# Optimization experiments

Measured on AMD Instinct MI355X. Metric: run time of the kernel, lower is better.

## Reference

```python
import jax, jax.numpy as jnp
import numpy as np

B, T, D_IN = 64, 1024, 400
H = 128            # hidden_dim_1 // 2 per direction
HD1, HD2 = 256, 64
N_CLASS, CONTEXT = 2, 2
EPS = 1e-5


def _lstm_dir(xs, w_ih, w_hh, b_ih, b_hh, reverse):
    # xs: [T, B, D]; torch gate order i, f, g, o
    Bd = xs.shape[1]
    def step(carry, xt):
        h, c = carry
        g = xt @ w_ih.T + b_ih + h @ w_hh.T + b_hh
        i, f, gg, o = jnp.split(g, 4, axis=-1)
        c = jax.nn.sigmoid(f) * c + jax.nn.sigmoid(i) * jnp.tanh(gg)
        h = jax.nn.sigmoid(o) * jnp.tanh(c)
        return (h, c), h
    init = (jnp.zeros((Bd, H), xs.dtype), jnp.zeros((Bd, H), xs.dtype))
    _, hs = jax.lax.scan(step, init, xs, reverse=reverse)
    return hs  # [T, B, H] in original time order


def _bn(x, g, b, m, v):  # eval-mode BatchNorm1d over last axis
    return (x - m) * jax.lax.rsqrt(v + EPS) * g + b


def _forward(x, w_ih_l0, w_hh_l0, b_ih_l0, b_hh_l0, w_ih_l0r, w_hh_l0r, b_ih_l0r, b_hh_l0r,
             w_ih_l1, w_hh_l1, b_ih_l1, b_hh_l1, w_ih_l1r, w_hh_l1r, b_ih_l1r, b_hh_l1r,
             bn1_g, bn1_b, bn1_m, bn1_v, lin_w, lin_b, bn2_g, bn2_b, bn2_m, bn2_v,
             out_w, out_b):
    xs = jnp.transpose(x, (1, 0, 2))  # [T, B, D_IN]
    # layer 0 bidirectional
    h_f = _lstm_dir(xs, w_ih_l0, w_hh_l0, b_ih_l0, b_hh_l0, False)
    h_b = _lstm_dir(xs, w_ih_l0r, w_hh_l0r, b_ih_l0r, b_hh_l0r, True)
    xs = jnp.concatenate([h_f, h_b], axis=-1)  # [T, B, 256]
    # layer 1 bidirectional
    h_f = _lstm_dir(xs, w_ih_l1, w_hh_l1, b_ih_l1, b_hh_l1, False)
    h_b = _lstm_dir(xs, w_ih_l1r, w_hh_l1r, b_ih_l1r, b_hh_l1r, True)
    lstm_out = jnp.concatenate([h_f, h_b], axis=-1)  # [T, B, 256]
    h = _bn(lstm_out, bn1_g, bn1_b, bn1_m, bn1_v)
    h = jnp.tanh(h @ lin_w.T + lin_b)
    h = _bn(h, bn2_g, bn2_b, bn2_m, bn2_v)  # [T, B, 64]
    # (equal x_len == T), so it is a per-batch scan with zero initial context
    def step(c, ht):  # c: [B, CONTEXT*N_CLASS], ht: [B, HD2]
        logits = jnp.concatenate([c, ht], axis=-1) @ out_w.T + out_b
        lo = jax.nn.log_softmax(logits, axis=-1)
        c_new = jax.lax.stop_gradient(jnp.concatenate([c[:, N_CLASS:], lo], axis=-1))
        return c_new, lo
    c0 = jnp.zeros((B, CONTEXT * N_CLASS), x.dtype)
    _, los = jax.lax.scan(step, c0, h)  # [T, B, N_CLASS]
    # torch flattens batch-major: row i = b * T + t
    return jnp.transpose(los, (1, 0, 2)).reshape(B * T, N_CLASS)


def setup_inputs() -> dict:
    keys = iter(jax.random.split(jax.random.key(0), 64))
    def u(shape):
        return jax.random.uniform(next(keys), shape, jnp.float32, -0.1, 0.1)
    inp = {"x": jax.random.normal(next(keys), (B, T, D_IN), jnp.float32)}
    for l, din in ((0, D_IN), (1, HD1)):
        for suf in ("", "r"):
            inp[f"w_ih_l{l}{suf}"] = u((4 * H, din))
            inp[f"w_hh_l{l}{suf}"] = u((4 * H, H))
            inp[f"b_ih_l{l}{suf}"] = u((4 * H,))
            inp[f"b_hh_l{l}{suf}"] = u((4 * H,))
    inp["bn1_g"] = u((HD1,)) + 1.0
    inp["bn1_b"] = u((HD1,))
    inp["bn1_m"] = u((HD1,))
    inp["bn1_v"] = jax.random.uniform(next(keys), (HD1,), jnp.float32, 0.5, 1.5)
    inp["lin_w"] = u((HD2, HD1))
    inp["lin_b"] = u((HD2,))
    inp["bn2_g"] = u((HD2,)) + 1.0
    inp["bn2_b"] = u((HD2,))
    inp["bn2_m"] = u((HD2,))
    inp["bn2_v"] = jax.random.uniform(next(keys), (HD2,), jnp.float32, 0.5, 1.5)
    inp["out_w"] = u((N_CLASS, CONTEXT * N_CLASS + HD2))
    inp["out_b"] = u((N_CLASS,))
    inp["x_len"] = jnp.full((B,), T, jnp.int32)
    return inp


def reference(x, w_ih_l0, w_hh_l0, b_ih_l0, b_hh_l0, w_ih_l0r, w_hh_l0r, b_ih_l0r, b_hh_l0r,
              w_ih_l1, w_hh_l1, b_ih_l1, b_hh_l1, w_ih_l1r, w_hh_l1r, b_ih_l1r, b_hh_l1r,
              bn1_g, bn1_b, bn1_m, bn1_v, lin_w, lin_b, bn2_g, bn2_b, bn2_m, bn2_v,
              out_w, out_b, x_len):
    # x_len is all-T (full-length sequences); packing is then a no-op and the
    # class_context reset indices coincide with sequence starts.
    return _forward(x, w_ih_l0, w_hh_l0, b_ih_l0, b_hh_l0, w_ih_l0r, w_hh_l0r, b_ih_l0r, b_hh_l0r,
                    w_ih_l1, w_hh_l1, b_ih_l1, b_hh_l1, w_ih_l1r, w_hh_l1r, b_ih_l1r, b_hh_l1r,
                    bn1_g, bn1_b, bn1_m, bn1_v, lin_w, lin_b, bn2_g, bn2_b, bn2_m, bn2_v,
                    out_w, out_b)
```

## Files before the change

### kernel.cpp

```cpp
#include <hip/hip_runtime.h>
#include <cstddef>
#include <cstdint>

#define T_LEN 1024
#define B_N   64
#define H_N   128
#define G_N   512
#define HD1_N 256
#define HD2_N 64
#define EPS_F 1e-5f

__device__ __forceinline__ unsigned short f2bf(float f) {
    unsigned int u = __float_as_uint(f);
    return (unsigned short)((u + 0x7FFFu + ((u >> 16) & 1u)) >> 16);
}
__device__ __forceinline__ float bf2f(unsigned short h) {
    return __uint_as_float(((unsigned int)h) << 16);
}

__global__ __launch_bounds__(256, 2)
void gemm_xp(const float* __restrict__ A,
             const float* __restrict__ w0, const float* __restrict__ w1,
             const float* __restrict__ bi0, const float* __restrict__ bh0,
             const float* __restrict__ bi1, const float* __restrict__ bh1,
             unsigned short* __restrict__ xp, int K, int a_is_x)
{
    const int mt = blockIdx.x, nt = blockIdx.y;
    const int m0 = mt * 128, n0 = nt * 128;
    const int dir = n0 >> 9;
    const int jj0 = n0 & 511;
    const float* __restrict__ W  = dir ? w1 : w0;
    const float* __restrict__ bi = dir ? bi1 : bi0;
    const float* __restrict__ bh = dir ? bh1 : bh0;
    const int tid = threadIdx.x;
    const int lr = tid >> 1;
    const int lc = (tid & 1) * 4;

    __shared__ __align__(16) float As[8][132];
    __shared__ __align__(16) float Bs[8][132];

    size_t arow;
    {
        int am = m0 + lr;
        if (a_is_x) { int t = am >> 6, b = am & 63; arow = ((size_t)b * T_LEN + t) * (size_t)K; }
        else        { arow = (size_t)am * (size_t)K; }
    }
    const size_t brow = (size_t)(jj0 + lr) * (size_t)K;

    float acc[8][8];
#pragma unroll
    for (int i = 0; i < 8; ++i)
#pragma unroll
        for (int j = 0; j < 8; ++j) acc[i][j] = 0.f;

    const int ty = tid >> 4, tx = tid & 15;

    for (int k0 = 0; k0 < K; k0 += 8) {
        float4 av = *(const float4*)(A + arow + k0 + lc);
        float4 bv = *(const float4*)(W + brow + k0 + lc);
        __syncthreads();
        As[lc+0][lr] = av.x; As[lc+1][lr] = av.y; As[lc+2][lr] = av.z; As[lc+3][lr] = av.w;
        Bs[lc+0][lr] = bv.x; Bs[lc+1][lr] = bv.y; Bs[lc+2][lr] = bv.z; Bs[lc+3][lr] = bv.w;
        __syncthreads();
#pragma unroll
        for (int kk = 0; kk < 8; ++kk) {
            float a[8], bb[8];
            float4 t0 = *(const float4*)&As[kk][ty*8];
            float4 t1 = *(const float4*)&As[kk][ty*8+4];
            a[0]=t0.x; a[1]=t0.y; a[2]=t0.z; a[3]=t0.w;
            a[4]=t1.x; a[5]=t1.y; a[6]=t1.z; a[7]=t1.w;
            float4 u0 = *(const float4*)&Bs[kk][tx*8];
            float4 u1 = *(const float4*)&Bs[kk][tx*8+4];
            bb[0]=u0.x; bb[1]=u0.y; bb[2]=u0.z; bb[3]=u0.w;
            bb[4]=u1.x; bb[5]=u1.y; bb[6]=u1.z; bb[7]=u1.w;
#pragma unroll
            for (int i = 0; i < 8; ++i)
#pragma unroll
                for (int j = 0; j < 8; ++j)
                    acc[i][j] += a[i] * bb[j];
        }
    }

    float bias[8];
#pragma unroll
    for (int j = 0; j < 8; ++j) {
        int jj = jj0 + tx*8 + j;
        bias[j] = bi[jj] + bh[jj];
    }
    const size_t outbase = (size_t)dir * (size_t)T_LEN * B_N * G_N;
#pragma unroll
    for (int i = 0; i < 8; ++i) {
        int m = m0 + ty*8 + i;
        unsigned int pk[4];
#pragma unroll
        for (int j = 0; j < 4; ++j) {
            unsigned short lo = f2bf(acc[i][2*j]   + bias[2*j]);
            unsigned short hi = f2bf(acc[i][2*j+1] + bias[2*j+1]);
            pk[j] = (unsigned int)lo | ((unsigned int)hi << 16);
        }
        unsigned short* op = xp + outbase + (size_t)m * G_N + jj0 + tx*8;
        *(uint4*)(op) = make_uint4(pk[0], pk[1], pk[2], pk[3]);
    }
}

__global__ __launch_bounds__(512, 2)
void lstm_scan(const unsigned short* __restrict__ xp,
               const float* __restrict__ whh_f, const float* __restrict__ whh_r,
               float* __restrict__ hout)
{
    const int tid = threadIdx.x;
    const int c   = tid & 127;
    const int rp  = tid >> 7;
    const int dir = blockIdx.x >> 6;
    const int b   = blockIdx.x & 63;
    const float* __restrict__ whh = dir ? whh_r : whh_f;
    const unsigned short* __restrict__ xpd =
        xp + (size_t)dir * T_LEN * B_N * G_N + (size_t)b * G_N;

    float w[4][32];
#pragma unroll
    for (int g = 0; g < 4; ++g) {
        const float* wr = whh + (size_t)(g * H_N + c) * H_N + rp * 32;
#pragma unroll
        for (int kk = 0; kk < 32; kk += 4) {
            float4 v = *(const float4*)(wr + kk);
            w[g][kk]=v.x; w[g][kk+1]=v.y; w[g][kk+2]=v.z; w[g][kk+3]=v.w;
        }
    }

    __shared__ __align__(16) float h_sh[128];
    __shared__ float part[4][4][128];
    __shared__ float gates_sh[512];

    if (tid < 128) h_sh[tid] = 0.f;
    float cst = 0.f;
    __syncthreads();

    float xpv = bf2f(xpd[(size_t)(dir ? (T_LEN-1) : 0) * B_N * G_N + tid]);

    for (int step = 0; step < T_LEN; ++step) {
        const int t = dir ? (T_LEN - 1 - step) : step;
        const int stepn = (step + 1 < T_LEN) ? step + 1 : step;
        const int tn = dir ? (T_LEN - 1 - stepn) : stepn;
        float xpn = bf2f(xpd[(size_t)tn * B_N * G_N + tid]);

        float a0=0.f, a1=0.f, a2=0.f, a3=0.f;
#pragma unroll
        for (int kk = 0; kk < 32; kk += 4) {
            float4 h4 = *(const float4*)&h_sh[rp*32 + kk];
            a0 += w[0][kk+0]*h4.x + w[0][kk+1]*h4.y + w[0][kk+2]*h4.z + w[0][kk+3]*h4.w;
            a1 += w[1][kk+0]*h4.x + w[1][kk+1]*h4.y + w[1][kk+2]*h4.z + w[1][kk+3]*h4.w;
            a2 += w[2][kk+0]*h4.x + w[2][kk+1]*h4.y + w[2][kk+2]*h4.z + w[2][kk+3]*h4.w;
            a3 += w[3][kk+0]*h4.x + w[3][kk+1]*h4.y + w[3][kk+2]*h4.z + w[3][kk+3]*h4.w;
        }
        part[0][rp][c]=a0; part[1][rp][c]=a1; part[2][rp][c]=a2; part[3][rp][c]=a3;
        __syncthreads();
        {
            float s = xpv + part[rp][0][c] + part[rp][1][c] + part[rp][2][c] + part[rp][3][c];
            float v;
            if (rp == 2) { float e = __expf(2.f*s); v = 1.f - 2.f/(e+1.f); }
            else         { v = 1.f / (1.f + __expf(-s)); }
            gates_sh[tid] = v;
        }
        __syncthreads();
        if (tid < 128) {
            float iv = gates_sh[tid];
            float fv = gates_sh[128+tid];
            float gv = gates_sh[256+tid];
            float ov = gates_sh[384+tid];
            cst = fv*cst + iv*gv;
            float e = __expf(2.f*cst);
            float th = 1.f - 2.f/(e+1.f);
            float hv = ov*th;
            h_sh[tid] = hv;
            hout[((size_t)t * B_N + b) * HD1_N + dir * H_N + tid] = hv;
        }
        xpv = xpn;
        __syncthreads();
    }
}

__global__ __launch_bounds__(256, 2)
void head_gemm(const float* __restrict__ A,
               const float* __restrict__ lin_w, const float* __restrict__ lin_b,
               const float* __restrict__ g1, const float* __restrict__ b1v,
               const float* __restrict__ m1, const float* __restrict__ v1,
               const float* __restrict__ g2, const float* __restrict__ b2v,
               const float* __restrict__ m2, const float* __restrict__ v2,
               float* __restrict__ h2out)
{
    const int m0 = blockIdx.x * 128;
    const int tid = threadIdx.x;
    __shared__ __align__(16) float As[8][132];
    __shared__ __align__(16) float Bs[8][68];
    const int lr  = tid >> 1, lc = (tid & 1) * 4;
    const int lrB = tid & 63, kcB = (tid >> 6) * 2;
    const int ty = tid >> 4, tx = tid & 15;

    float acc[8][4];
#pragma unroll
    for (int i = 0; i < 8; ++i)
#pragma unroll
        for (int j = 0; j < 4; ++j) acc[i][j] = 0.f;

    const size_t arow = (size_t)(m0 + lr) * HD1_N;
    for (int k0 = 0; k0 < HD1_N; k0 += 8) {
        float4 av = *(const float4*)(A + arow + k0 + lc);
        float4 gm = *(const float4*)(m1 + k0 + lc);
        float4 gg = *(const float4*)(g1 + k0 + lc);
        float4 gv = *(const float4*)(v1 + k0 + lc);
        float2 bv = *(const float2*)(lin_w + (size_t)lrB * HD1_N + k0 + kcB);
        __syncthreads();
        As[lc+0][lr] = (av.x - gm.x) * (gg.x * rsqrtf(gv.x + EPS_F));
        As[lc+1][lr] = (av.y - gm.y) * (gg.y * rsqrtf(gv.y + EPS_F));
        As[lc+2][lr] = (av.z - gm.z) * (gg.z * rsqrtf(gv.z + EPS_F));
        As[lc+3][lr] = (av.w - gm.w) * (gg.w * rsqrtf(gv.w + EPS_F));
        Bs[kcB][lrB]   = bv.x;
        Bs[kcB+1][lrB] = bv.y;
        __syncthreads();
#pragma unroll
        for (int kk = 0; kk < 8; ++kk) {
            float a[8], bb[4];
            float4 t0 = *(const float4*)&As[kk][ty*8];
            float4 t1 = *(const float4*)&As[kk][ty*8+4];
            a[0]=t0.x; a[1]=t0.y; a[2]=t0.z; a[3]=t0.w;
            a[4]=t1.x; a[5]=t1.y; a[6]=t1.z; a[7]=t1.w;
            float4 u0 = *(const float4*)&Bs[kk][tx*4];
            bb[0]=u0.x; bb[1]=u0.y; bb[2]=u0.z; bb[3]=u0.w;
#pragma unroll
            for (int i = 0; i < 8; ++i)
#pragma unroll
                for (int j = 0; j < 4; ++j)
                    acc[i][j] += a[i] * bb[j];
        }
    }

#pragma unroll
    for (int j = 0; j < 4; ++j) {
        int n = tx*4 + j;
        float s2 = g2[n] * rsqrtf(v2[n] + EPS_F);
        float t2 = b2v[n] - m2[n] * s2;
        float lb = lin_b[n];
#pragma unroll
        for (int i = 0; i < 8; ++i) {
            float y = acc[i][j] + lb;
            acc[i][j] = tanhf(y) * s2 + t2;
        }
    }
#pragma unroll
    for (int i = 0; i < 8; ++i) {
        int m = m0 + ty*8 + i;
        float4 o;
        o.x = acc[i][0]; o.y = acc[i][1]; o.z = acc[i][2]; o.w = acc[i][3];
        *(float4*)(h2out + (size_t)m * HD2_N + tx*4) = o;
    }
}

__global__ __launch_bounds__(256)
void hw_kernel(const float* __restrict__ h2, const float* __restrict__ out_w,
               const float* __restrict__ out_b, float* __restrict__ hw)
{
    int m = blockIdx.x * blockDim.x + threadIdx.x;
    const float* w0 = out_w + 4;
    const float* w1 = out_w + 68 + 4;
    float a0 = out_b[0], a1 = out_b[1];
    const float* row = h2 + (size_t)m * HD2_N;
#pragma unroll
    for (int j = 0; j < 64; j += 4) {
        float4 hv = *(const float4*)(row + j);
        a0 += hv.x*w0[j] + hv.y*w0[j+1] + hv.z*w0[j+2] + hv.w*w0[j+3];
        a1 += hv.x*w1[j] + hv.y*w1[j+1] + hv.z*w1[j+2] + hv.w*w1[j+3];
    }
    *(float2*)(hw + (size_t)m * 2) = make_float2(a0, a1);
}

__global__ void ctx_kernel(const float* __restrict__ hw,
                           const float* __restrict__ out_w,
                           float* __restrict__ out)
{
    int b = threadIdx.x;
    float w00=out_w[0],  w01=out_w[1],  w02=out_w[2],  w03=out_w[3];
    float w10=out_w[68], w11=out_w[69], w12=out_w[70], w13=out_w[71];
    float c0=0.f, c1=0.f, c2=0.f, c3=0.f;
    float2 buf[8];
#pragma unroll
    for (int u = 0; u < 8; ++u)
        buf[u] = *(const float2*)&hw[((size_t)u * B_N + b) * 2];
    for (int tb = 0; tb < T_LEN; tb += 8) {
#pragma unroll
        for (int u = 0; u < 8; ++u) {
            int t = tb + u;
            float2 hv = buf[u];
            int tnext = t + 8;
            if (tnext < T_LEN)
                buf[u] = *(const float2*)&hw[((size_t)tnext * B_N + b) * 2];
            float l0 = hv.x + c0*w00 + c1*w01 + c2*w02 + c3*w03;
            float l1 = hv.y + c0*w10 + c1*w11 + c2*w12 + c3*w13;
            float mx = fmaxf(l0, l1);
            float lse = mx + __logf(__expf(l0 - mx) + __expf(l1 - mx));
            l0 -= lse; l1 -= lse;
            c0 = c2; c1 = c3; c2 = l0; c3 = l1;
            *(float2*)&out[((size_t)b * T_LEN + t) * 2] = make_float2(l0, l1);
        }
    }
}

extern "C" void kernel_launch(void* const* d_in, const int* in_sizes, int n_in,
                              void* d_out, int out_size, void* d_ws, size_t ws_size,
                              hipStream_t stream)
{
    (void)in_sizes; (void)n_in; (void)out_size; (void)ws_size;
    const float* x        = (const float*)d_in[0];
    const float* w_ih_l0  = (const float*)d_in[1];
    const float* w_hh_l0  = (const float*)d_in[2];
    const float* b_ih_l0  = (const float*)d_in[3];
    const float* b_hh_l0  = (const float*)d_in[4];
    const float* w_ih_l0r = (const float*)d_in[5];
    const float* w_hh_l0r = (const float*)d_in[6];
    const float* b_ih_l0r = (const float*)d_in[7];
    const float* b_hh_l0r = (const float*)d_in[8];
    const float* w_ih_l1  = (const float*)d_in[9];
    const float* w_hh_l1  = (const float*)d_in[10];
    const float* b_ih_l1  = (const float*)d_in[11];
    const float* b_hh_l1  = (const float*)d_in[12];
    const float* w_ih_l1r = (const float*)d_in[13];
    const float* w_hh_l1r = (const float*)d_in[14];
    const float* b_ih_l1r = (const float*)d_in[15];
    const float* b_hh_l1r = (const float*)d_in[16];
    const float* bn1_g = (const float*)d_in[17];
    const float* bn1_b = (const float*)d_in[18];
    const float* bn1_m = (const float*)d_in[19];
    const float* bn1_v = (const float*)d_in[20];
    const float* lin_w = (const float*)d_in[21];
    const float* lin_b = (const float*)d_in[22];
    const float* bn2_g = (const float*)d_in[23];
    const float* bn2_b = (const float*)d_in[24];
    const float* bn2_m = (const float*)d_in[25];
    const float* bn2_v = (const float*)d_in[26];
    const float* out_w = (const float*)d_in[27];
    const float* out_b = (const float*)d_in[28];
    float* out = (float*)d_out;

    unsigned short* xp = (unsigned short*)d_ws;
    float* l0out = (float*)((char*)d_ws + 134217728);
    float* l1out = l0out;
    float* h2    = (float*)d_ws;
    float* hw    = h2 + 4194304;

    dim3 gg(512, 8);
    gemm_xp<<<gg, 256, 0, stream>>>(x, w_ih_l0, w_ih_l0r, b_ih_l0, b_hh_l0,
                                    b_ih_l0r, b_hh_l0r, xp, 400, 1);
    lstm_scan<<<128, 512, 0, stream>>>(xp, w_hh_l0, w_hh_l0r, l0out);
    gemm_xp<<<gg, 256, 0, stream>>>(l0out, w_ih_l1, w_ih_l1r, b_ih_l1, b_hh_l1,
                                    b_ih_l1r, b_hh_l1r, xp, 256, 0);
    lstm_scan<<<128, 512, 0, stream>>>(xp, w_hh_l1, w_hh_l1r, l1out);
    head_gemm<<<512, 256, 0, stream>>>(l1out, lin_w, lin_b,
                                       bn1_g, bn1_b, bn1_m, bn1_v,
                                       bn2_g, bn2_b, bn2_m, bn2_v, h2);
    hw_kernel<<<256, 256, 0, stream>>>(h2, out_w, out_b, hw);
    ctx_kernel<<<1, 64, 0, stream>>>(hw, out_w, out);
}
```

Baseline: 3.058 ms.

## Restructure LSTM scan to one barrier per step using DPP and shuffles

The recurrent scan now uses 1024 threads per block. Each pair of lanes computes one gate row's dot product over half of the hidden vector and combines the halves with a DPP swap. The four gates for a hidden unit are gathered with wave shuffles, and h is double-buffered in shared memory, so each step needs one barrier instead of three and no partial-sum or gate arrays in shared memory. The projected-input buffer also switches from bf16 to fp16, which changes rounding and range, and the larger block may raise register pressure.

Measured after the change: 3.945 ms. 29.0% more time.

```diff
diff --git a/kernel.cpp b/kernel.cpp
--- a/kernel.cpp
+++ b/kernel.cpp
@@ -10,12 +10,18 @@
 #define HD2_N 64
 #define EPS_F 1e-5f
 
-__device__ __forceinline__ unsigned short f2bf(float f) {
-    unsigned int u = __float_as_uint(f);
-    return (unsigned short)((u + 0x7FFFu + ((u >> 16) & 1u)) >> 16);
-}
-__device__ __forceinline__ float bf2f(unsigned short h) {
-    return __uint_as_float(((unsigned int)h) << 16);
+typedef _Float16 half_t;
+typedef half_t half2_t __attribute__((ext_vector_type(2)));
+
+__device__ __forceinline__ float h2f(unsigned short u) {
+    half_t h = __builtin_bit_cast(half_t, u);
+    return (float)h;
+}
+
+template<int CTRL>
+__device__ __forceinline__ float dppf(float v) {
+    return __int_as_float(
+        __builtin_amdgcn_mov_dpp(__float_as_int(v), CTRL, 0xF, 0xF, true));
 }
 
 __global__ __launch_bounds__(256, 2)
@@ -94,88 +100,91 @@
         unsigned int pk[4];
 #pragma unroll
         for (int j = 0; j < 4; ++j) {
-            unsigned short lo = f2bf(acc[i][2*j]   + bias[2*j]);
-            unsigned short hi = f2bf(acc[i][2*j+1] + bias[2*j+1]);
-            pk[j] = (unsigned int)lo | ((unsigned int)hi << 16);
+            half2_t hp = { (half_t)(acc[i][2*j]   + bias[2*j]),
+                           (half_t)(acc[i][2*j+1] + bias[2*j+1]) };
+            pk[j] = __builtin_bit_cast(unsigned int, hp);
         }
         unsigned short* op = xp + outbase + (size_t)m * G_N + jj0 + tx*8;
         *(uint4*)(op) = make_uint4(pk[0], pk[1], pk[2], pk[3]);
     }
 }
 
-__global__ __launch_bounds__(512, 2)
+__global__ __launch_bounds__(1024, 4)
 void lstm_scan(const unsigned short* __restrict__ xp,
                const float* __restrict__ whh_f, const float* __restrict__ whh_r,
                float* __restrict__ hout)
 {
-    const int tid = threadIdx.x;
-    const int c   = tid & 127;
-    const int rp  = tid >> 7;
+    const int tid  = threadIdx.x;
+    const int c    = tid >> 3;
+    const int g    = (tid >> 1) & 3;
+    const int half = tid & 1;
     const int dir = blockIdx.x >> 6;
     const int b   = blockIdx.x & 63;
     const float* __restrict__ whh = dir ? whh_r : whh_f;
+    const int j = g * H_N + c;
     const unsigned short* __restrict__ xpd =
-        xp + (size_t)dir * T_LEN * B_N * G_N + (size_t)b * G_N;
-
-    float w[4][32];
-#pragma unroll
-    for (int g = 0; g < 4; ++g) {
-        const float* wr = whh + (size_t)(g * H_N + c) * H_N + rp * 32;
-#pragma unroll
-        for (int kk = 0; kk < 32; kk += 4) {
-            float4 v = *(const float4*)(wr + kk);
-            w[g][kk]=v.x; w[g][kk+1]=v.y; w[g][kk+2]=v.z; w[g][kk+3]=v.w;
-        }
-    }
-
-    __shared__ __align__(16) float h_sh[128];
-    __shared__ float part[4][4][128];
-    __shared__ float gates_sh[512];
-
-    if (tid < 128) h_sh[tid] = 0.f;
+        xp + (size_t)dir * T_LEN * B_N * G_N + (size_t)b * G_N + j;
+
+    float2 w2[32];
+    {
+        const float* wr = whh + (size_t)j * H_N + half * 64;
+#pragma unroll
+        for (int d = 0; d < 16; ++d) {
+            float4 v = *(const float4*)(wr + 4*d);
+            w2[2*d]   = make_float2(v.x, v.y);
+            w2[2*d+1] = make_float2(v.z, v.w);
+        }
+    }
+
+    __shared__ __align__(16) float hbuf[2][128];
+    if (tid < 128) hbuf[0][tid] = 0.f;
     float cst = 0.f;
     __syncthreads();
 
-    float xpv = bf2f(xpd[(size_t)(dir ? (T_LEN-1) : 0) * B_N * G_N + tid]);
+    int cur = 0;
+    float xpv = h2f(xpd[(size_t)(dir ? (T_LEN - 1) : 0) * B_N * G_N]);
+
+    const int lane = tid & 63;
+    const int base = lane & 56;
 
     for (int step = 0; step < T_LEN; ++step) {
-        const int t = dir ? (T_LEN - 1 - step) : step;
-        const int stepn = (step + 1 < T_LEN) ? step + 1 : step;
-        const int tn = dir ? (T_LEN - 1 - stepn) : stepn;
-        float xpn = bf2f(xpd[(size_t)tn * B_N * G_N + tid]);
-
-        float a0=0.f, a1=0.f, a2=0.f, a3=0.f;
-#pragma unroll
-        for (int kk = 0; kk < 32; kk += 4) {
-            float4 h4 = *(const float4*)&h_sh[rp*32 + kk];
-            a0 += w[0][kk+0]*h4.x + w[0][kk+1]*h4.y + w[0][kk+2]*h4.z + w[0][kk+3]*h4.w;
-            a1 += w[1][kk+0]*h4.x + w[1][kk+1]*h4.y + w[1][kk+2]*h4.z + w[1][kk+3]*h4.w;
-            a2 += w[2][kk+0]*h4.x + w[2][kk+1]*h4.y + w[2][kk+2]*h4.z + w[2][kk+3]*h4.w;
-            a3 += w[3][kk+0]*h4.x + w[3][kk+1]*h4.y + w[3][kk+2]*h4.z + w[3][kk+3]*h4.w;
-        }
-        part[0][rp][c]=a0; part[1][rp][c]=a1; part[2][rp][c]=a2; part[3][rp][c]=a3;
-        __syncthreads();
-        {
-            float s = xpv + part[rp][0][c] + part[rp][1][c] + part[rp][2][c] + part[rp][3][c];
-            float v;
-            if (rp == 2) { float e = __expf(2.f*s); v = 1.f - 2.f/(e+1.f); }
-            else         { v = 1.f / (1.f + __expf(-s)); }
-            gates_sh[tid] = v;
-        }
-        __syncthreads();
-        if (tid < 128) {
-            float iv = gates_sh[tid];
-            float fv = gates_sh[128+tid];
-            float gv = gates_sh[256+tid];
-            float ov = gates_sh[384+tid];
-            cst = fv*cst + iv*gv;
-            float e = __expf(2.f*cst);
-            float th = 1.f - 2.f/(e+1.f);
-            float hv = ov*th;
-            h_sh[tid] = hv;
-            hout[((size_t)t * B_N + b) * HD1_N + dir * H_N + tid] = hv;
+        const int t  = dir ? (T_LEN - 1 - step) : step;
+        const int sn = (step + 1 < T_LEN) ? step + 1 : step;
+        const int tn = dir ? (T_LEN - 1 - sn) : sn;
+        float xpn = h2f(xpd[(size_t)tn * B_N * G_N]);
+
+        float ax = 0.f, ay = 0.f;
+        const float* hp = &hbuf[cur][half * 64];
+#pragma unroll
+        for (int d = 0; d < 16; ++d) {
+            float4 h4 = *(const float4*)(hp + 4*d);
+            ax += w2[2*d].x   * h4.x;  ay += w2[2*d].y   * h4.y;
+            ax += w2[2*d+1].x * h4.z;  ay += w2[2*d+1].y * h4.w;
+        }
+        float a = ax + ay;
+        a += dppf<0xB1>(a);
+        float s = a + xpv;
+
+        float in_v = (g == 2) ? 2.f * s : s;
+        float sg = 1.f / (1.f + __expf(-in_v));
+        float act = (g == 2) ? 2.f * sg - 1.f : sg;
+
+        float iv = __shfl(act, base + 0, 64);
+        float fv = __shfl(act, base + 2, 64);
+        float gv = __shfl(act, base + 4, 64);
+        float ov = __shfl(act, base + 6, 64);
+
+        cst = fv * cst + iv * gv;
+        float e2 = __expf(2.f * cst);
+        float th = 1.f - 2.f / (e2 + 1.f);
+        float hv = ov * th;
+
+        if ((tid & 7) == 0) {
+            hbuf[cur ^ 1][c] = hv;
+            hout[((size_t)t * B_N + b) * HD1_N + dir * H_N + c] = hv;
         }
         xpv = xpn;
+        cur ^= 1;
         __syncthreads();
     }
 }
@@ -350,10 +359,10 @@
     dim3 gg(512, 8);
     gemm_xp<<<gg, 256, 0, stream>>>(x, w_ih_l0, w_ih_l0r, b_ih_l0, b_hh_l0,
                                     b_ih_l0r, b_hh_l0r, xp, 400, 1);
-    lstm_scan<<<128, 512, 0, stream>>>(xp, w_hh_l0, w_hh_l0r, l0out);
+    lstm_scan<<<128, 1024, 0, stream>>>(xp, w_hh_l0, w_hh_l0r, l0out);
     gemm_xp<<<gg, 256, 0, stream>>>(l0out, w_ih_l1, w_ih_l1r, b_ih_l1, b_hh_l1,
                                     b_ih_l1r, b_hh_l1r, xp, 256, 0);
-    lstm_scan<<<128, 512, 0, stream>>>(xp, w_hh_l1, w_hh_l1r, l1out);
+    lstm_scan<<<128, 1024, 0, stream>>>(xp, w_hh_l1, w_hh_l1r, l1out);
     head_gemm<<<512, 256, 0, stream>>>(l1out, lin_w, lin_b,
                                        bn1_g, bn1_b, bn1_m, bn1_v,
                                        bn2_g, bn2_b, bn2_m, bn2_v, h2);
```
